# Performance work log

Hardware: AMD Instinct MI355X
Metric: run time of the kernel (lower is better)

Reference implementation:

```python
import jax, jax.numpy as jnp
import numpy as np

B, T1, T2 = 2, 1024, 512
D_MODEL, N_HEAD, D_HEAD = 1024, 16, 64
SCALE = 1.0 / D_HEAD ** 0.5
EPS = 1e-5


def _skew(qe):
    # qe: [B, H, T, 2T-1] -> [B, H, T, T] via Transformer-XL pad/reshape trick
    b, h, t, x = qe.shape
    qe = jnp.pad(qe, ((0, 0), (0, 0), (0, 0), (0, 1))).reshape(b, h, 2 * t * t)
    qe = jnp.pad(qe, ((0, 0), (0, 0), (0, t - 1))).reshape(b, h, t + 1, 2 * t - 1)
    return qe[:, :, :t, -t:]


def setup_inputs() -> dict:
    key = jax.random.key(0)
    ks = jax.random.split(key, 12)
    s = 0.02
    return {
        "Q": jax.random.normal(ks[0], (B, T1, D_MODEL), jnp.float32),
        "K": jax.random.normal(ks[1], (B, T1, D_MODEL), jnp.float32),
        "V": jax.random.normal(ks[2], (B, T1, D_MODEL), jnp.float32),
        "lookup_table": jax.random.normal(ks[3], (2 * T1 - 1, D_HEAD), jnp.float32) * s,
        "valid_frames": jnp.sort(jax.random.randint(ks[4], (T2,), 0, T1)),
        "mask": jax.random.bernoulli(ks[5], 0.1, (B, N_HEAD, T1, T2)),
        "Wq": jax.random.normal(ks[6], (D_MODEL, N_HEAD * D_HEAD), jnp.float32) * s,
        "Wk": jax.random.normal(ks[7], (D_MODEL, N_HEAD * D_HEAD), jnp.float32) * s,
        "Wv": jax.random.normal(ks[8], (D_MODEL, N_HEAD * D_HEAD), jnp.float32) * s,
        "Wo": jax.random.normal(ks[9], (N_HEAD * D_HEAD, D_MODEL), jnp.float32) * s,
        "bo": jnp.zeros((D_MODEL,), jnp.float32),
        "ln_g": jnp.ones((D_MODEL,), jnp.float32),
        "ln_b": jnp.zeros((D_MODEL,), jnp.float32),
    }


def reference(Q, K, V, lookup_table, valid_frames, mask, Wq, Wk, Wv, Wo, bo, ln_g, ln_b):
    # gather valid KV frames (raw inputs, before projection)
    K = K[:, valid_frames]  # [B, T2, D]
    V = V[:, valid_frames]
    # pre-layernorm on Q only
    mu = jnp.mean(Q, axis=-1, keepdims=True)
    var = jnp.var(Q, axis=-1, keepdims=True)
    Qn = (Q - mu) * jax.lax.rsqrt(var + EPS) * ln_g + ln_b
    # projections -> [B, H, T, d_head]
    q = (Qn @ Wq).reshape(B, T1, N_HEAD, D_HEAD).transpose(0, 2, 1, 3)
    k = (K @ Wk).reshape(B, T2, N_HEAD, D_HEAD).transpose(0, 2, 1, 3)
    v = (V @ Wv).reshape(B, T2, N_HEAD, D_HEAD).transpose(0, 2, 1, 3)
    # content score + skewed relative-position score
    score = jnp.einsum("bhqd,bhkd->bhqk", q, k)  # [B,H,T1,T2]
    rel = jnp.einsum("bhqd,xd->bhqx", q, lookup_table)  # [B,H,T1,2T1-1]
    rel = _skew(rel)[:, :, :, valid_frames]  # [B,H,T1,T2]
    score = (score + rel) * SCALE
    score = jnp.where(mask, -jnp.finfo(score.dtype).max, score)
    attn = jax.nn.softmax(score, axis=-1)
    ctx = jnp.einsum("bhqk,bhkd->bhqd", attn, v)
    ctx = ctx.transpose(0, 2, 1, 3).reshape(B, T1, N_HEAD * D_HEAD)
    out = ctx @ Wo + bo  # dropout is identity at inference
    return out + ctx  # pre_layernorm=True branch
```

## Files before the change

kernel.cpp:

```cpp
#include <hip/hip_runtime.h>
#include <stdint.h>
#include <stddef.h>

typedef __attribute__((ext_vector_type(8))) short s16x8;
typedef __attribute__((ext_vector_type(4))) short s16x4;
typedef __attribute__((ext_vector_type(4))) float f32x4;
typedef __attribute__((ext_vector_type(2))) unsigned int u32x2;

#define MFMA(a,b,c) __builtin_amdgcn_mfma_f32_16x16x32_bf16((a),(b),(c),0,0,0)

static __device__ __forceinline__ unsigned short f2b(float f){
  unsigned int b = __float_as_uint(f);
  b = (b + 0x7FFFu + ((b>>16)&1u)) >> 16;
  return (unsigned short)b;
}
static __device__ __forceinline__ float b2f(unsigned short u){
  return __uint_as_float(((unsigned int)u)<<16);
}


__global__ __launch_bounds__(256) void k_prep(
    const float* __restrict__ Q, const float* __restrict__ g, const float* __restrict__ be,
    unsigned short* __restrict__ Qn,
    const float* __restrict__ K, const float* __restrict__ V, const int* __restrict__ vf,
    unsigned short* __restrict__ Kg, unsigned short* __restrict__ Vg,
    const float* __restrict__ L, unsigned short* __restrict__ Lb,
    const float* __restrict__ W0, const float* __restrict__ W1,
    const float* __restrict__ W2, const float* __restrict__ W3,
    unsigned short* __restrict__ D0, unsigned short* __restrict__ D1,
    unsigned short* __restrict__ D2, unsigned short* __restrict__ D3,
    const unsigned char* __restrict__ mkb, unsigned int* __restrict__ MB){
  __shared__ float tile[64][65];
  __shared__ float red[8];
  __shared__ int cnt1, cnt23;
  const int bid = blockIdx.x, t = threadIdx.x;
  if(bid < 2048){
    const float4* xp = (const float4*)(Q + (size_t)bid*1024);
    float4 v = xp[t];
    float s  = v.x+v.y+v.z+v.w;
    float s2 = v.x*v.x+v.y*v.y+v.z*v.z+v.w*v.w;
    #pragma unroll
    for(int o=1;o<64;o<<=1){ s += __shfl_xor(s,o); s2 += __shfl_xor(s2,o); }
    int w = t>>6, l = t&63;
    if(l==0){ red[w]=s; red[4+w]=s2; }
    __syncthreads();
    s  = red[0]+red[1]+red[2]+red[3];
    s2 = red[4]+red[5]+red[6]+red[7];
    float mu = s*(1.f/1024.f);
    float var = s2*(1.f/1024.f) - mu*mu;
    float rs = rsqrtf(var + 1e-5f);
    float4 gv = ((const float4*)g)[t];
    float4 bv = ((const float4*)be)[t];
    ushort4 o4;
    o4.x = f2b((v.x-mu)*rs*gv.x + bv.x);
    o4.y = f2b((v.y-mu)*rs*gv.y + bv.y);
    o4.z = f2b((v.z-mu)*rs*gv.z + bv.z);
    o4.w = f2b((v.w-mu)*rs*gv.w + bv.w);
    ((ushort4*)(Qn + (size_t)bid*1024))[t] = o4;
  } else if(bid < 4096){
    int row = bid - 2048;
    int isV = row>>10, r = row&1023;
    int b = r>>9, jj = r&511;
    const float* src = (isV? V : K) + ((size_t)(b*1024 + vf[jj]))*1024;
    unsigned short* dst = (isV? Vg : Kg) + (size_t)r*1024;
    float4 v = ((const float4*)src)[t];
    ushort4 o; o.x=f2b(v.x); o.y=f2b(v.y); o.z=f2b(v.z); o.w=f2b(v.w);
    ((ushort4*)dst)[t] = o;
  } else if(bid < 4608){
    int i = (bid-4096)*256 + t;
    if(i < 2047*64) Lb[i] = f2b(L[i]);
  } else if(bid < 5632){
    int idx = bid - 4608;
    int z = idx>>8, rem = idx&255;
    int k0 = (rem&15)*64, n0 = (rem>>4)*64;
    const float* S = z==0?W0: z==1?W1: z==2?W2:W3;
    unsigned short* D = z==0?D0: z==1?D1: z==2?D2:D3;
    int tr = t>>6, tc = t&63;
    #pragma unroll
    for(int it=0;it<16;it++){ int r = it*4+tr; tile[r][tc] = S[(size_t)(k0+r)*1024 + n0+tc]; }
    __syncthreads();
    #pragma unroll
    for(int it=0;it<16;it++){ int r = it*4+tr; D[(size_t)(n0+r)*1024 + k0+tc] = f2b(tile[tc][r]); }
  } else {
    const int mb = bid - 5632;
    const size_t g0 = (size_t)mb*16;
    if(t==0){ cnt1=0; cnt23=0; }
    __syncthreads();
    const uint4* bp = (const uint4*)(mkb + g0*512);
    int l1=0,l23=0;
    #pragma unroll
    for(int i=0;i<2;i++){
      uint4 v = bp[t + i*256];
      unsigned int ws[4] = {v.x,v.y,v.z,v.w};
      #pragma unroll
      for(int j=0;j<4;j++){
        if((ws[j]>>8)&0xFFu) l1++;
        if(ws[j]>>16)        l23++;
      }
    }
    #pragma unroll
    for(int o=1;o<64;o<<=1){ l1 += __shfl_xor(l1,o); l23 += __shfl_xor(l23,o); }
    if((t&63)==0){ atomicAdd(&cnt1,l1); atomicAdd(&cnt23,l23); }
    __syncthreads();
    const int flag = cnt1 ? 1 : (cnt23 ? 2 : 0);
    const int rl = t>>4, f = t&15;
    const size_t base = (g0 + rl)*512 + f;
    unsigned int word = 0;
    if(flag==0){
      const int* p = (const int*)mkb;
      #pragma unroll
      for(int i=0;i<32;i++) word |= (p[base+i*16]!=0 ? 1u:0u) << i;
    } else if(flag==1){
      #pragma unroll
      for(int i=0;i<32;i++) word |= (mkb[base+i*16]!=0 ? 1u:0u) << i;
    } else {
      const float* p = (const float*)mkb;
      #pragma unroll
      for(int i=0;i<32;i++) word |= (p[base+i*16]!=0.f ? 1u:0u) << i;
    }
    MB[((size_t)mb*4 + (t>>6))*64 + f*4 + (rl&3)] = word;
  }
}

__global__ __launch_bounds__(256) void k_proj(
    const short* __restrict__ QN, const short* __restrict__ WQT,
    const short* __restrict__ KG, const short* __restrict__ WKT,
    const short* __restrict__ WVT, const short* __restrict__ VG,
    unsigned short* __restrict__ QB, unsigned short* __restrict__ KB,
    unsigned short* __restrict__ VT){
  __shared__ __align__(16) short Ab[64*32];
  __shared__ __align__(16) short Bb[128*32];
  int bid = blockIdx.x;
  int mode, bx;
  if(bid<256){ mode=0; bx=bid>>3; }
  else if(bid<384){ mode=1; bx=(bid-256)>>3; }
  else { mode=2; bx=(bid-384)>>3; }
  int by = bid&7;
  const short* A  = mode==0? QN : mode==1? KG : WVT;
  const short* Bt = mode==0? WQT: mode==1? WKT: VG;

  const int t = threadIdx.x;
  const int w = t>>6, l = t&63;
  const int fl15 = l&15, fl4 = l>>4;
  const size_t m0 = (size_t)bx*64, n0 = (size_t)by*128;
  const int srow = t>>2, scb = t&3;
  const int sg = scb ^ ((srow>>1)&3);
  const short* Ap = A + (m0+srow)*1024 + 8*sg;
  const short* Bp = Bt + (n0+srow)*1024 + 8*sg;

  f32x4 acc[4][2];
  const f32x4 zero = {0.f,0.f,0.f,0.f};
  #pragma unroll
  for(int m=0;m<4;m++)
    #pragma unroll
    for(int n=0;n<2;n++) acc[m][n] = zero;

  for(int k0=0;k0<1024;k0+=32){
    s16x8 a0 = *(const s16x8*)(Ap + k0);
    s16x8 b0 = *(const s16x8*)(Bp + k0);
    s16x8 b1 = *(const s16x8*)(Bp + 64*1024 + k0);
    __syncthreads();
    *(s16x8*)(Ab + srow*32 + scb*8)      = a0;
    *(s16x8*)(Bb + srow*32 + scb*8)      = b0;
    *(s16x8*)(Bb + (64+srow)*32 + scb*8) = b1;
    __syncthreads();
    s16x8 af[4], bff[2];
    #pragma unroll
    for(int m=0;m<4;m++){
      int row = m*16 + fl15;
      int gg = fl4 ^ ((row>>1)&3);
      af[m] = *(const s16x8*)(Ab + row*32 + gg*8);
    }
    #pragma unroll
    for(int n=0;n<2;n++){
      int row = w*32 + n*16 + fl15;
      int gg = fl4 ^ ((row>>1)&3);
      bff[n] = *(const s16x8*)(Bb + row*32 + gg*8);
    }
    #pragma unroll
    for(int m=0;m<4;m++)
      #pragma unroll
      for(int n=0;n<2;n++)
        acc[m][n] = MFMA(af[m], bff[n], acc[m][n]);
  }

  #pragma unroll
  for(int m=0;m<4;m++){
    #pragma unroll
    for(int n=0;n<2;n++){
      int mgb = (int)m0 + m*16 + 4*fl4;
      int ng  = (int)n0 + w*32 + n*16 + fl15;
      #pragma unroll
      for(int p=0;p<4;p++){
        int mg = mgb + p;
        float v = acc[m][n][p];
        if(mode==0){ int b=mg>>10, i=mg&1023, h=ng>>6, d=ng&63;
          QB[((size_t)((b*16+h)*1024+i))*64 + d] = f2b(v); }
        else if(mode==1){ int b=mg>>9, jj=mg&511, h=ng>>6, d=ng&63;
          KB[((size_t)((b*16+h)*512+jj))*64 + d] = f2b(v); }
        else { int h=mg>>6, d=mg&63, b=ng>>9, jj=ng&511;
          VT[((size_t)((b*16+h)*64+d))*512 + jj] = f2b(v); }
      }
    }
  }
}

__global__ __launch_bounds__(256) void k_gemmO(
    const short* __restrict__ A, const short* __restrict__ Bt,
    float* __restrict__ out, const float* __restrict__ bo,
    const float* __restrict__ ctxf){
  __shared__ __align__(16) short Ab[64*32];
  __shared__ __align__(16) short Bb[128*32];
  const int bid = blockIdx.x;
  const int bx = bid>>3, by = bid&7;
  const int t = threadIdx.x;
  const int w = t>>6, l = t&63;
  const int fl15 = l&15, fl4 = l>>4;
  const size_t m0 = (size_t)bx*64, n0 = (size_t)by*128;
  const int srow = t>>2, scb = t&3;
  const int sg = scb ^ ((srow>>1)&3);
  const short* Ap = A + (m0+srow)*1024 + 8*sg;
  const short* Bp = Bt + (n0+srow)*1024 + 8*sg;

  f32x4 acc[4][2];
  const f32x4 zero = {0.f,0.f,0.f,0.f};
  #pragma unroll
  for(int m=0;m<4;m++)
    #pragma unroll
    for(int n=0;n<2;n++) acc[m][n] = zero;

  for(int k0=0;k0<1024;k0+=32){
    s16x8 a0 = *(const s16x8*)(Ap + k0);
    s16x8 b0 = *(const s16x8*)(Bp + k0);
    s16x8 b1 = *(const s16x8*)(Bp + 64*1024 + k0);
    __syncthreads();
    *(s16x8*)(Ab + srow*32 + scb*8)      = a0;
    *(s16x8*)(Bb + srow*32 + scb*8)      = b0;
    *(s16x8*)(Bb + (64+srow)*32 + scb*8) = b1;
    __syncthreads();
    s16x8 af[4], bff[2];
    #pragma unroll
    for(int m=0;m<4;m++){
      int row = m*16 + fl15;
      int gg = fl4 ^ ((row>>1)&3);
      af[m] = *(const s16x8*)(Ab + row*32 + gg*8);
    }
    #pragma unroll
    for(int n=0;n<2;n++){
      int row = w*32 + n*16 + fl15;
      int gg = fl4 ^ ((row>>1)&3);
      bff[n] = *(const s16x8*)(Bb + row*32 + gg*8);
    }
    #pragma unroll
    for(int m=0;m<4;m++)
      #pragma unroll
      for(int n=0;n<2;n++)
        acc[m][n] = MFMA(af[m], bff[n], acc[m][n]);
  }

  #pragma unroll
  for(int m=0;m<4;m++){
    #pragma unroll
    for(int n=0;n<2;n++){
      int mgb = (int)m0 + m*16 + 4*fl4;
      int ng  = (int)n0 + w*32 + n*16 + fl15;
      #pragma unroll
      for(int p=0;p<4;p++){
        int mg = mgb + p;
        size_t idx = (size_t)mg*1024 + ng;
        out[idx] = acc[m][n][p] + bo[ng] + ctxf[idx];
      }
    }
  }
}

#define G_RGS 20
#define G_ROWS 272
__global__ __launch_bounds__(512,4) void k_attn(const short* __restrict__ qb,
    const short* __restrict__ kb, const short* __restrict__ vt,
    const short* __restrict__ lbf, const int* __restrict__ vf,
    const unsigned int* __restrict__ MB,
    unsigned short* __restrict__ ctxb, float* __restrict__ ctxf){
  __shared__ __align__(16) short Gs[4][G_ROWS*G_RGS];
  __shared__ int vfs[512];
  const int t=threadIdx.x, w=t>>6, l=t&63, fl15=l&15, fl4=l>>4;
  const int logical = ((blockIdx.x & 7) << 8) + (blockIdx.x >> 3);
  const int bh = logical >> 6;
  const int qg = logical & 63;
  const int qw = qg*16;

  const short* qp = qb + ((size_t)(bh*1024 + qw + fl15))*64 + 8*fl4;
  s16x8 qa0 = *(const s16x8*)qp;
  s16x8 qa1 = *(const s16x8*)(qp+32);
  const int rowgrp = bh*256 + qg*4 + fl4;
  uint4 mv = ((const uint4*)MB)[rowgrp*16 + fl15];

  const short* kp_row = kb + ((size_t)(bh*512 + fl15))*64 + 8*fl4;
  s16x8 kf[8];
  #pragma unroll
  for(int i=0;i<4;i++){
    const short* ka = kp_row + (size_t)(4*w+i)*1024;
    kf[2*i]   = *(const s16x8*)ka;
    kf[2*i+1] = *(const s16x8*)(ka+32);
  }

  vfs[t] = vf[t & 511];
  __syncthreads();
  const int vf0 = vfs[0];
  const int x0  = 1008 + vf0 - qw;
  const int cw  = w&3;
  const int xcw = x0 + cw*256;

  short* Gw = &Gs[cw][0];
  const f32x4 zero = {0.f,0.f,0.f,0.f};
  const int tbeg = (w>>2)? 9 : 0;
  const int tend = (w>>2)? 17 : 9;
  for(int tt=tbeg; tt<tend; tt++){
    int xr = xcw + tt*16 + fl15; if(xr>2046) xr = 2046;
    const short* lp = lbf + (size_t)xr*64 + 8*fl4;
    s16x8 b0 = *(const s16x8*)lp;
    s16x8 b1 = *(const s16x8*)(lp+32);
    f32x4 a = zero;
    a = MFMA(qa0,b0,a); a = MFMA(qa1,b1,a);
    u32x2 pk;
    pk.x = (unsigned int)f2b(a[0]) | ((unsigned int)f2b(a[1])<<16);
    pk.y = (unsigned int)f2b(a[2]) | ((unsigned int)f2b(a[3])<<16);
    int u = tt*16 + fl15;
    *(u32x2*)(Gw + u*G_RGS + 4*fl4) = pk;
  }

  unsigned int mbits[4] = {mv.x, mv.y, mv.z, mv.w};
  __syncthreads();

  short rlv[4][4];
  #pragma unroll
  for(int i=0;i<4;i++){
    int jj = (4*w+i)*16 + fl15;
    int o  = vfs[jj] - vf0;
    const short* gc = &Gs[o>>8][((o&255)+15)*G_RGS - 76*fl4];
    #pragma unroll
    for(int p=0;p<4;p++) rlv[i][p] = gc[-19*p];
  }
  __syncthreads();

  f32x4 S[4];
  #pragma unroll
  for(int tl=0;tl<4;tl++){
    int ttg = 4*w + tl;
    f32x4 a = zero;
    a = MFMA(qa0, kf[2*tl], a); a = MFMA(qa1, kf[2*tl+1], a);
    #pragma unroll
    for(int p=0;p<4;p++){
      float sv = (a[p] + b2f((unsigned short)rlv[tl][p])) * 0.125f;
      bool mskb = (mbits[p]>>ttg)&1u;
      a[p] = mskb ? -1e30f : sv;
    }
    S[tl] = a;
  }

  const short* vpb[4];
  #pragma unroll
  for(int dt=0;dt<4;dt++)
    vpb[dt] = vt + ((size_t)(bh*64 + dt*16 + fl15))*512 + w*64 + 8*fl4;
  s16x8 vfr[8];
  #pragma unroll
  for(int dt=0;dt<4;dt++){
    vfr[2*dt]   = *(const s16x8*)(vpb[dt]);
    vfr[2*dt+1] = *(const s16x8*)(vpb[dt] + 32);
  }

  float m_run[4], ps[4];
  #pragma unroll
  for(int p=0;p<4;p++){
    float cm = fmaxf(fmaxf(S[0][p],S[1][p]), fmaxf(S[2][p],S[3][p]));
    #pragma unroll
    for(int o=1;o<16;o<<=1) cm = fmaxf(cm, __shfl_xor(cm,o));
    m_run[p] = cm;
    ps[p] = 0.f;
  }
  short* Pw = ((short*)Gs) + w*1024;
  #pragma unroll
  for(int tl=0;tl<4;tl++){
    int col = (tl*16 + fl15) ^ (fl4<<4);
    #pragma unroll
    for(int p=0;p<4;p++){
      float e = __expf(S[tl][p]-m_run[p]);
      ps[p] += e;
      Pw[(4*fl4+p)*64 + col] = (short)f2b(e);
    }
  }
  f32x4 facc[4];
  #pragma unroll
  for(int dt=0;dt<4;dt++) facc[dt] = zero;
  #pragma unroll
  for(int s=0;s<2;s++){
    s16x8 pa = *(const s16x8*)(Pw + fl15*64 + ((s*32 + fl4*8) ^ ((fl15>>2)<<4)));
    #pragma unroll
    for(int dt=0;dt<4;dt++)
      facc[dt] = MFMA(pa, vfr[2*dt+s], facc[dt]);
  }

  #pragma unroll
  for(int p=0;p<4;p++){
    #pragma unroll
    for(int o=1;o<16;o<<=1) ps[p] += __shfl_xor(ps[p],o);
  }

  __syncthreads();
  float* MT = (float*)&Gs[0][0];
  float* ST = MT + 128;
  float* MG = (float*)(((char*)&Gs[0][0]) + 1024);
  if(fl15==0){
    #pragma unroll
    for(int p=0;p<4;p++){ MT[w*16 + 4*fl4+p] = m_run[p]; ST[w*16 + 4*fl4+p] = ps[p]; }
  }
  __syncthreads();
  float scale[4];
  #pragma unroll
  for(int p=0;p<4;p++){
    int row = 4*fl4+p;
    float ms = -1e30f;
    #pragma unroll
    for(int k=0;k<8;k++) ms = fmaxf(ms, MT[k*16+row]);
    float den = 0.f;
    #pragma unroll
    for(int k=0;k<8;k++) den += __expf(MT[k*16+row]-ms)*ST[k*16+row];
    scale[p] = __expf(m_run[p]-ms) / den;
  }
  #pragma unroll
  for(int dt=0;dt<4;dt++){
    f32x4 v4;
    #pragma unroll
    for(int p=0;p<4;p++) v4[p] = facc[dt][p]*scale[p];
    *(f32x4*)&MG[((w*4+dt)*16 + fl15)*20 + 4*fl4] = v4;
  }
  __syncthreads();
  if(w < 4){
    const int b = bh>>4, h = bh&15;
    f32x4 vs = zero;
    #pragma unroll
    for(int k=0;k<8;k++)
      vs += *(const f32x4*)&MG[((k*4+w)*16 + fl15)*20 + 4*fl4];
    #pragma unroll
    for(int p=0;p<4;p++){
      int row = 4*fl4+p;
      size_t idx = ((size_t)(b*1024 + qw + row))*1024 + h*64 + w*16 + fl15;
      ctxb[idx] = f2b(vs[p]);
      ctxf[idx] = vs[p];
    }
  }
}

extern "C" void kernel_launch(void* const* d_in, const int* in_sizes, int n_in,
                              void* d_out, int out_size, void* d_ws, size_t ws_size,
                              hipStream_t stream){
  (void)in_sizes; (void)n_in; (void)out_size; (void)ws_size;
  const float* Q  = (const float*)d_in[0];
  const float* K  = (const float*)d_in[1];
  const float* V  = (const float*)d_in[2];
  const float* Lt = (const float*)d_in[3];
  const int*   vf = (const int*)d_in[4];
  const void*  mk = d_in[5];
  const float* Wq = (const float*)d_in[6];
  const float* Wk = (const float*)d_in[7];
  const float* Wv = (const float*)d_in[8];
  const float* Wo = (const float*)d_in[9];
  const float* bo = (const float*)d_in[10];
  const float* lg = (const float*)d_in[11];
  const float* lb = (const float*)d_in[12];

  char* base = (char*)d_ws;
  size_t off = 0;
  auto alloc = [&](size_t bytes)->char*{
    char* p = base + off; off += (bytes + 255) & ~(size_t)255; return p; };
  unsigned int*   MBp = (unsigned int*)alloc(32768ull*16*4);
  unsigned short* QN  = (unsigned short*)alloc(2048ull*1024*2);
  unsigned short* KG  = (unsigned short*)alloc(1024ull*1024*2);
  unsigned short* VG  = (unsigned short*)alloc(1024ull*1024*2);
  unsigned short* WQT = (unsigned short*)alloc(1024ull*1024*2);
  unsigned short* WKT = (unsigned short*)alloc(1024ull*1024*2);
  unsigned short* WVT = (unsigned short*)alloc(1024ull*1024*2);
  unsigned short* WOT = (unsigned short*)alloc(1024ull*1024*2);
  unsigned short* LB  = (unsigned short*)alloc(2047ull*64*2);
  unsigned short* QB  = (unsigned short*)alloc(32ull*1024*64*2);
  unsigned short* KB  = (unsigned short*)alloc(32ull*512*64*2);
  unsigned short* VT  = (unsigned short*)alloc(32ull*64*512*2);
  unsigned short* CB  = (unsigned short*)alloc(2048ull*1024*2);
  float*          CF  = (float*)alloc(2048ull*1024*4);

  k_prep<<<7680,256,0,stream>>>(Q, lg, lb, QN, K, V, vf, KG, VG, Lt, LB,
                                Wq, Wk, Wv, Wo, WQT, WKT, WVT, WOT,
                                (const unsigned char*)mk, MBp);
  k_proj<<<512,256,0,stream>>>((const short*)QN,(const short*)WQT,
                               (const short*)KG,(const short*)WKT,
                               (const short*)WVT,(const short*)VG,
                               QB, KB, VT);
  k_attn<<<2048,512,0,stream>>>((const short*)QB,(const short*)KB,(const short*)VT,
                                (const short*)LB, vf, MBp, CB, CF);
  k_gemmO<<<256,256,0,stream>>>((const short*)CB,(const short*)WOT,
                                (float*)d_out, bo, CF);
}
```

Baseline: 134.5 us.

## Drop vfs LDS staging and a barrier; defer softmax rescale to reducer

Valid-frame offsets are now loaded from global memory straight into registers, which removes the shared vfs array and one block barrier. The cross-wave softmax merge no longer scales partial outputs in every wave before a second barrier. Waves write raw accumulators and the four reducer waves compute max, denominator and weights while summing. Launch bounds rise from 4 to 6 blocks per CU, which forces fewer registers per thread and risks spills.

```diff
diff --git a/kernel.cpp b/kernel.cpp
--- a/kernel.cpp
+++ b/kernel.cpp
@@ -276,13 +276,12 @@
 
 #define G_RGS 20
 #define G_ROWS 272
-__global__ __launch_bounds__(512,4) void k_attn(const short* __restrict__ qb,
+__global__ __launch_bounds__(512,6) void k_attn(const short* __restrict__ qb,
     const short* __restrict__ kb, const short* __restrict__ vt,
     const short* __restrict__ lbf, const int* __restrict__ vf,
     const unsigned int* __restrict__ MB,
     unsigned short* __restrict__ ctxb, float* __restrict__ ctxf){
   __shared__ __align__(16) short Gs[4][G_ROWS*G_RGS];
-  __shared__ int vfs[512];
   const int t=threadIdx.x, w=t>>6, l=t&63, fl15=l&15, fl4=l>>4;
   const int logical = ((blockIdx.x & 7) << 8) + (blockIdx.x >> 3);
   const int bh = logical >> 6;
@@ -303,10 +302,11 @@
     kf[2*i]   = *(const s16x8*)ka;
     kf[2*i+1] = *(const s16x8*)(ka+32);
   }
-
-  vfs[t] = vf[t & 511];
-  __syncthreads();
-  const int vf0 = vfs[0];
+  const int vf0 = vf[0];
+  int ov[4];
+  #pragma unroll
+  for(int i=0;i<4;i++) ov[i] = vf[(4*w+i)*16 + fl15] - vf0;
+
   const int x0  = 1008 + vf0 - qw;
   const int cw  = w&3;
   const int xcw = x0 + cw*256;
@@ -335,8 +335,7 @@
   short rlv[4][4];
   #pragma unroll
   for(int i=0;i<4;i++){
-    int jj = (4*w+i)*16 + fl15;
-    int o  = vfs[jj] - vf0;
+    int o = ov[i];
     const short* gc = &Gs[o>>8][((o&255)+15)*G_RGS - 76*fl4];
     #pragma unroll
     for(int p=0;p<4;p++) rlv[i][p] = gc[-19*p];
@@ -414,39 +413,43 @@
     #pragma unroll
     for(int p=0;p<4;p++){ MT[w*16 + 4*fl4+p] = m_run[p]; ST[w*16 + 4*fl4+p] = ps[p]; }
   }
-  __syncthreads();
-  float scale[4];
-  #pragma unroll
-  for(int p=0;p<4;p++){
-    int row = 4*fl4+p;
-    float ms = -1e30f;
-    #pragma unroll
-    for(int k=0;k<8;k++) ms = fmaxf(ms, MT[k*16+row]);
-    float den = 0.f;
-    #pragma unroll
-    for(int k=0;k<8;k++) den += __expf(MT[k*16+row]-ms)*ST[k*16+row];
-    scale[p] = __expf(m_run[p]-ms) / den;
-  }
-  #pragma unroll
-  for(int dt=0;dt<4;dt++){
-    f32x4 v4;
-    #pragma unroll
-    for(int p=0;p<4;p++) v4[p] = facc[dt][p]*scale[p];
-    *(f32x4*)&MG[((w*4+dt)*16 + fl15)*20 + 4*fl4] = v4;
-  }
+  #pragma unroll
+  for(int dt=0;dt<4;dt++)
+    *(f32x4*)&MG[((w*4+dt)*16 + fl15)*20 + 4*fl4] = facc[dt];
   __syncthreads();
   if(w < 4){
-    const int b = bh>>4, h = bh&15;
-    f32x4 vs = zero;
-    #pragma unroll
-    for(int k=0;k<8;k++)
-      vs += *(const f32x4*)&MG[((k*4+w)*16 + fl15)*20 + 4*fl4];
+    float ms[4], den[4], ek[8][4];
     #pragma unroll
     for(int p=0;p<4;p++){
       int row = 4*fl4+p;
+      float m = -1e30f;
+      #pragma unroll
+      for(int k=0;k<8;k++) m = fmaxf(m, MT[k*16+row]);
+      ms[p] = m;
+      float d = 0.f;
+      #pragma unroll
+      for(int k=0;k<8;k++){
+        float e = __expf(MT[k*16+row]-m);
+        ek[k][p] = e;
+        d += e*ST[k*16+row];
+      }
+      den[p] = d;
+    }
+    f32x4 vs = zero;
+    #pragma unroll
+    for(int k=0;k<8;k++){
+      f32x4 raw = *(const f32x4*)&MG[((k*4+w)*16 + fl15)*20 + 4*fl4];
+      #pragma unroll
+      for(int p=0;p<4;p++) vs[p] += ek[k][p]*raw[p];
+    }
+    const int b = bh>>4, h = bh&15;
+    #pragma unroll
+    for(int p=0;p<4;p++){
+      float v = vs[p] / den[p];
+      int row = 4*fl4+p;
       size_t idx = ((size_t)(b*1024 + qw + row))*1024 + h*64 + w*16 + fl15;
-      ctxb[idx] = f2b(vs[p]);
-      ctxf[idx] = vs[p];
+      ctxb[idx] = f2b(v);
+      ctxf[idx] = v;
     }
   }
 }
```

New measurement: 133.7 us. No clear change (-0.6%).
